# Kernel tuning notes

Hardware: AMD Instinct MI355X
Metric: run time of the kernel (lower is better)

The kernel has to match this reference:

```python
import jax, jax.numpy as jnp
import numpy as np
from jax import lax

B, T, D = 4, 4096, 1024
H = 16                 # n_heads
HD = D // H            # head_dim = 64
NS = 64                # num_slots
SPH = NS // H          # slots_per_head = 4
KPH = 2                # effective per-head top_k = min(max(2, 32//16), 4) = 2
K = KPH * H            # total topk width = 32
HM = 4096              # hidden_mlp


def _p(key, shape, scale=0.02):
    return jax.random.normal(key, shape, dtype=jnp.float32) * scale


def setup_inputs() -> dict:
    key = jax.random.key(0)
    ks = jax.random.split(key, 24)
    return {
        "x": jax.random.normal(ks[0], (B, T, D), dtype=jnp.float32),
        "slot_init": _p(ks[1], (H, SPH, HD)),
        # route_mlp: Linear(2D, D) -> GELU -> Linear(D, NS); weights stored [in, out]
        "rw1": _p(ks[2], (2 * D, D)), "rb1": jnp.zeros((D,), jnp.float32),
        "rw2": _p(ks[3], (D, NS)), "rb2": jnp.zeros((NS,), jnp.float32),
        # GRUCell(HD, HD): torch layout [3*HD, HD]
        "gwi": _p(ks[4], (3 * HD, HD), 0.1), "gwh": _p(ks[5], (3 * HD, HD), 0.1),
        "gbi": jnp.zeros((3 * HD,), jnp.float32), "gbh": jnp.zeros((3 * HD,), jnp.float32),
        # slot_hidden_proj: Linear(HD, 4*HD); slot_out_head: Linear(4*HD, HD)
        "hpw": _p(ks[6], (HD, 4 * HD)), "hpb": jnp.zeros((4 * HD,), jnp.float32),
        "ohw": _p(ks[7], (4 * HD, HD)), "ohb": jnp.zeros((HD,), jnp.float32),
        # slot_value_proj: Linear(D, HM); slot_value_out: Linear(HM, D)
        "vpw": _p(ks[8], (D, HM)), "vpb": jnp.zeros((HM,), jnp.float32),
        "vow": _p(ks[9], (HM, D)), "vob": jnp.zeros((D,), jnp.float32),
        # out_proj: Linear(D, D)
        "opw": _p(ks[10], (D, D)), "opb": jnp.zeros((D,), jnp.float32),
        "tau": jnp.ones((1,), jnp.float32),
    }


def _gelu(x):
    return jax.nn.gelu(x, approximate=False)


def _forward(x, slot_init, rw1, rb1, rw2, rb2, gwi, gwh, gbi, gbh,
             hpw, hpb, ohw, ohb, vpw, vpb, vow, vob, opw, opb, tau):
    # ---- routing ----
    S0 = slot_init.reshape(NS, HD)                     # [NS, HD]
    slot_mean = S0.mean(axis=0)                        # [HD]
    slot_mean_full = jnp.tile(slot_mean, H)            # [D]
    ctx = jnp.concatenate(
        [x, jnp.broadcast_to(slot_mean_full, (B, T, D))], axis=-1)  # [B,T,2D]
    h1 = _gelu(ctx @ rw1 + rb1)
    route_logits = (h1 @ rw2 + rb2) / (jnp.abs(tau[0]) + 0.1)       # [B,T,NS]

    topk_vals, topk_idx = lax.top_k(route_logits, K)   # [B,T,K]
    topk_w = jax.nn.softmax(topk_vals, axis=-1)
    bi = jnp.arange(B)[:, None, None]
    ti = jnp.arange(T)[None, :, None]
    alpha = jnp.zeros((B, T, NS), x.dtype).at[bi, ti, topk_idx].set(topk_w)

    # ---- per-head slot pooling (vectorized over heads) ----
    alpha_h = alpha.reshape(B, T, H, SPH)              # [B,T,H,S]
    x_heads = x.reshape(B, T, H, HD)                   # [B,T,H,HD]
    slot_input = jnp.einsum('bths,bthd->bhsd', alpha_h, x_heads)   # [B,H,S,HD]
    wsum = alpha_h.sum(axis=1) + 1e-8                  # [B,H,S]
    slot_in = slot_input / wsum[..., None]

    # ---- GRU cell update (torch GRUCell semantics) ----
    h_prev = jnp.broadcast_to(slot_init[None], (B, H, SPH, HD))
    gi = slot_in @ gwi.T + gbi                         # [B,H,S,3HD]
    gh = h_prev @ gwh.T + gbh
    ir, iz, in_ = jnp.split(gi, 3, axis=-1)
    hr, hz, hn = jnp.split(gh, 3, axis=-1)
    r = jax.nn.sigmoid(ir + hr)
    z = jax.nn.sigmoid(iz + hz)
    n = jnp.tanh(in_ + r * hn)
    h_new = (1.0 - z) * n + z * h_prev                 # [B,H,S,HD]

    S_new = _gelu(h_new @ hpw + hpb) @ ohw + ohb       # [B,H,S,HD]

    # ---- broadcast back to tokens ----
    out = jnp.einsum('bths,bhsd->bthd', alpha_h, S_new).reshape(B, T, D)
    out = _gelu(out @ vpw + vpb) @ vow + vob
    out = out @ opw + opb
    return out


def reference(x, slot_init, rw1, rb1, rw2, rb2, gwi, gwh, gbi, gbh,
              hpw, hpb, ohw, ohb, vpw, vpb, vow, vob, opw, opb, tau):
    return _forward(x, slot_init, rw1, rb1, rw2, rb2, gwi, gwh, gbi, gbh,
                    hpw, hpb, ohw, ohb, vpw, vpb, vow, vob, opw, opb, tau)
```

## Files before the change

kernel.cpp:

```cpp
#include <hip/hip_runtime.h>
#include <cstddef>
#include <cstdint>

#define Bb 4
#define Tt 4096
#define Dd 1024
#define Hh 16
#define HDd 64
#define NSs 64
#define SPHh 4
#define HMm 4096
#define MTOK (Bb*Tt)

typedef _Float16 f16x8 __attribute__((ext_vector_type(8)));
typedef _Float16 f16x4 __attribute__((ext_vector_type(4)));
typedef float f32x4 __attribute__((ext_vector_type(4)));

__device__ __forceinline__ float gelu_f(float x) {
    return 0.5f * x * (1.0f + erff(x * 0.70710678118654752440f));
}

__device__ __forceinline__ int xcd_swz(int nwg) {
    int orig = blockIdx.y * gridDim.x + blockIdx.x;
    int cpx = nwg >> 3;
    return (orig & 7) * cpx + (orig >> 3);
}

__global__ __launch_bounds__(256) void cb_part_k(const float* __restrict__ slot_init,
                                                 const float* __restrict__ rw1,
                                                 float* __restrict__ cbp) {
    __shared__ float sm[64];
    int tid = threadIdx.x;
    if (tid < 64) {
        float s = 0.f;
        for (int i = 0; i < 64; ++i) s += slot_init[i * 64 + tid];
        sm[tid] = s * (1.0f / 64.0f);
    }
    __syncthreads();
    int j = blockIdx.x * 256 + tid;
    int k0 = blockIdx.y * 64;
    float acc = 0.f;
#pragma unroll 8
    for (int k = 0; k < 64; ++k)
        acc = fmaf(sm[k], rw1[(size_t)(1024 + k0 + k) * 1024 + j], acc);
    cbp[(size_t)blockIdx.y * 1024 + j] = acc;
}

__global__ __launch_bounds__(256) void cb_comb_k(const float* __restrict__ cbp,
                                                 float* __restrict__ cb) {
    int j = blockIdx.x * 256 + threadIdx.x;
    float acc = 0.f;
#pragma unroll
    for (int c = 0; c < 16; ++c) acc += cbp[(size_t)c * 1024 + j];
    cb[j] = acc;
}

__global__ __launch_bounds__(256) void wsplitT_k(const float* __restrict__ rw1,
                                                 _Float16* __restrict__ whiT,
                                                 _Float16* __restrict__ wloT) {
    __shared__ float t[32][33];
    int n0 = blockIdx.x * 32, k0 = blockIdx.y * 32;
    int tx = threadIdx.x & 31, ty = threadIdx.x >> 5;
#pragma unroll
    for (int i = 0; i < 32; i += 8)
        t[ty + i][tx] = rw1[(size_t)(k0 + ty + i) * 1024 + n0 + tx];
    __syncthreads();
#pragma unroll
    for (int i = 0; i < 32; i += 8) {
        float v = t[tx][ty + i];
        _Float16 h = (_Float16)v;
        _Float16 l = (_Float16)(v - (float)h);
        whiT[(size_t)(n0 + ty + i) * 1024 + k0 + tx] = h;
        wloT[(size_t)(n0 + ty + i) * 1024 + k0 + tx] = l;
    }
}

__global__ __launch_bounds__(256) void xsplit_k(const float* __restrict__ x,
                                                _Float16* __restrict__ xhi,
                                                _Float16* __restrict__ xlo) {
    size_t i = ((size_t)blockIdx.x * 256 + threadIdx.x) * 8;
    float4 a = *(const float4*)(x + i);
    float4 b = *(const float4*)(x + i + 4);
    float v[8] = {a.x, a.y, a.z, a.w, b.x, b.y, b.z, b.w};
    f16x8 h, l;
#pragma unroll
    for (int j = 0; j < 8; ++j) {
        _Float16 hv = (_Float16)v[j];
        h[j] = hv;
        l[j] = (_Float16)(v[j] - (float)hv);
    }
    *(f16x8*)(xhi + i) = h;
    *(f16x8*)(xlo + i) = l;
}

__global__ __launch_bounds__(256) void hgemm4_k(const _Float16* __restrict__ Ah,
                                                const _Float16* __restrict__ Al,
                                                const _Float16* __restrict__ Bh,
                                                const _Float16* __restrict__ Bl,
                                                const float* __restrict__ bias1,
                                                const float* __restrict__ bias2,
                                                float* __restrict__ C,
                                                int M, int N, int K) {
    __shared__ __align__(16) _Float16 Ahs[128][32];
    __shared__ __align__(16) _Float16 Als[128][32];
    __shared__ __align__(16) _Float16 Bhs[128][32];
    __shared__ __align__(16) _Float16 Bls[128][32];
    const int tid = threadIdx.x;
    const int wid = tid >> 6;
    const int lane = tid & 63;
    const int swz = xcd_swz(gridDim.x * gridDim.y);
    const int brow = (swz / gridDim.x) * 128;
    const int bcol = (swz % gridDim.x) * 128;
    const int wr = (wid >> 1) * 64;
    const int wc = (wid & 1) * 64;

    const int rb = lane >> 2;
    const int cbk = (lane & 3) * 8;
    const int fr = lane & 15;
    const int fk = (lane >> 4) * 8;

    f32x4 acc[4][4];
#pragma unroll
    for (int m = 0; m < 4; ++m)
#pragma unroll
        for (int n = 0; n < 4; ++n)
            acc[m][n] = f32x4{0.f, 0.f, 0.f, 0.f};

    for (int k0 = 0; k0 < K; k0 += 32) {
#pragma unroll
        for (int i = 0; i < 2; ++i) {
            int r0 = wid * 32 + i * 16;
            const _Float16* gah = Ah + (size_t)(brow + r0 + rb) * K + k0 + cbk;
            __builtin_amdgcn_global_load_lds(
                (const __attribute__((address_space(1))) void*)gah,
                (__attribute__((address_space(3))) void*)&Ahs[r0][0], 16, 0, 0);
            const _Float16* gal = Al + (size_t)(brow + r0 + rb) * K + k0 + cbk;
            __builtin_amdgcn_global_load_lds(
                (const __attribute__((address_space(1))) void*)gal,
                (__attribute__((address_space(3))) void*)&Als[r0][0], 16, 0, 0);
            const _Float16* gbh = Bh + (size_t)(bcol + r0 + rb) * K + k0 + cbk;
            __builtin_amdgcn_global_load_lds(
                (const __attribute__((address_space(1))) void*)gbh,
                (__attribute__((address_space(3))) void*)&Bhs[r0][0], 16, 0, 0);
            const _Float16* gbl = Bl + (size_t)(bcol + r0 + rb) * K + k0 + cbk;
            __builtin_amdgcn_global_load_lds(
                (const __attribute__((address_space(1))) void*)gbl,
                (__attribute__((address_space(3))) void*)&Bls[r0][0], 16, 0, 0);
        }
        __syncthreads();

        f16x8 afh[4], afl[4], bfh[4], bfl[4];
#pragma unroll
        for (int m = 0; m < 4; ++m) {
            afh[m] = *(const f16x8*)&Ahs[wr + m * 16 + fr][fk];
            afl[m] = *(const f16x8*)&Als[wr + m * 16 + fr][fk];
        }
#pragma unroll
        for (int n = 0; n < 4; ++n) {
            bfh[n] = *(const f16x8*)&Bhs[wc + n * 16 + fr][fk];
            bfl[n] = *(const f16x8*)&Bls[wc + n * 16 + fr][fk];
        }
#pragma unroll
        for (int m = 0; m < 4; ++m)
#pragma unroll
            for (int n = 0; n < 4; ++n) {
                acc[m][n] = __builtin_amdgcn_mfma_f32_16x16x32_f16(afl[m], bfh[n], acc[m][n], 0, 0, 0);
                acc[m][n] = __builtin_amdgcn_mfma_f32_16x16x32_f16(afh[m], bfl[n], acc[m][n], 0, 0, 0);
                acc[m][n] = __builtin_amdgcn_mfma_f32_16x16x32_f16(afh[m], bfh[n], acc[m][n], 0, 0, 0);
            }
        __syncthreads();
    }

    const int crow = (lane >> 4) * 4;
#pragma unroll
    for (int m = 0; m < 4; ++m) {
        int row0 = brow + wr + m * 16 + crow;
#pragma unroll
        for (int n = 0; n < 4; ++n) {
            int col = bcol + wc + n * 16 + fr;
            float bv = bias1[col] + bias2[col];
#pragma unroll
            for (int r = 0; r < 4; ++r) {
                float v = acc[m][n][r] + bv;
                C[(size_t)(row0 + r) * N + col] = gelu_f(v);
            }
        }
    }
}

__global__ __launch_bounds__(256) void logits2_k(const float* __restrict__ A,
                                                 const float* __restrict__ Bw,
                                                 const float* __restrict__ rb2,
                                                 const float* __restrict__ taup,
                                                 float* __restrict__ Cl) {
    __shared__ float At[16][68];
    __shared__ float Bs[16][64];
    const int tid = threadIdx.x;
    const int m0 = blockIdx.x * 64;
    const int rg = tid >> 4;
    const int cg = tid & 15;
    const int srow = tid >> 2;
    const int skk  = (tid & 3) * 4;
    const int bk = tid >> 4;
    const int bc = (tid & 15) * 4;

    float acc[4][4] = {};

    for (int k0 = 0; k0 < 1024; k0 += 16) {
        float4 av = *(const float4*)(A + (size_t)(m0 + srow) * 1024 + k0 + skk);
        float4 bv = *(const float4*)(Bw + (size_t)(k0 + bk) * 64 + bc);
        __syncthreads();
        At[skk + 0][srow] = av.x;
        At[skk + 1][srow] = av.y;
        At[skk + 2][srow] = av.z;
        At[skk + 3][srow] = av.w;
        *(float4*)&Bs[bk][bc] = bv;
        __syncthreads();
#pragma unroll
        for (int k = 0; k < 16; ++k) {
            float4 a4 = *(const float4*)&At[k][rg * 4];
            float4 b4 = *(const float4*)&Bs[k][cg * 4];
            float a[4] = {a4.x, a4.y, a4.z, a4.w};
            float b[4] = {b4.x, b4.y, b4.z, b4.w};
#pragma unroll
            for (int i = 0; i < 4; ++i)
#pragma unroll
                for (int j = 0; j < 4; ++j)
                    acc[i][j] = fmaf(a[i], b[j], acc[i][j]);
        }
    }
    float inv = 1.0f / (fabsf(taup[0]) + 0.1f);
#pragma unroll
    for (int i = 0; i < 4; ++i)
#pragma unroll
        for (int j = 0; j < 4; ++j)
            Cl[(size_t)(m0 + rg * 4 + i) * 64 + cg * 4 + j] =
                (acc[i][j] + rb2[cg * 4 + j]) * inv;
}

__global__ __launch_bounds__(256) void topk_k(const float* __restrict__ logits,
                                              float* __restrict__ alpha,
                                              _Float16* __restrict__ alpha16) {
    int wave = threadIdx.x >> 6;
    int lane = threadIdx.x & 63;
    int t = blockIdx.x * 4 + wave;
    float li = logits[(size_t)t * 64 + lane];
    float m = li;
#pragma unroll
    for (int off = 32; off; off >>= 1) m = fmaxf(m, __shfl_xor(m, off, 64));
    int cnt = 0;
    for (int off = 1; off < 64; ++off) {
        int j = (lane + off) & 63;
        float lj = __shfl(li, j, 64);
        cnt += (lj > li) || (lj == li && j < lane);
    }
    float e = (cnt < 32) ? expf(li - m) : 0.0f;
    float s = e;
#pragma unroll
    for (int off = 32; off; off >>= 1) s += __shfl_xor(s, off, 64);
    float a = e / s;
    alpha[(size_t)t * 64 + lane] = a;
    alpha16[(size_t)t * 64 + lane] = (_Float16)a;
}

__global__ __launch_bounds__(256) void pool_part_k(const float* __restrict__ x,
                                                   const float* __restrict__ alpha,
                                                   float* __restrict__ part,
                                                   float* __restrict__ partw) {
    int bh = blockIdx.x;
    int c = blockIdx.y;
    int b = bh >> 4, h = bh & 15;
    int tid = threadIdx.x;
    int s = tid >> 6, d = tid & 63;
    __shared__ float lx[16][64];
    __shared__ float la[16][4];
    float acc = 0.f, wacc = 0.f;
    const int tchunk = Tt / 8;
    const int t0base = c * tchunk;
    for (int t0 = 0; t0 < tchunk; t0 += 16) {
        int ttr = tid >> 4;
        int ddr = (tid & 15) * 4;
        size_t trow = (size_t)b * Tt + t0base + t0 + ttr;
        float4 xv = *(const float4*)(x + trow * Dd + h * 64 + ddr);
        *(float4*)&lx[ttr][ddr] = xv;
        if (tid < 64) {
            int tt2 = tid >> 2, ss = tid & 3;
            la[tt2][ss] = alpha[((size_t)b * Tt + t0base + t0 + tt2) * 64 + h * 4 + ss];
        }
        __syncthreads();
#pragma unroll
        for (int q = 0; q < 16; ++q) {
            float av = la[q][s];
            acc = fmaf(av, lx[q][d], acc);
            wacc += av;
        }
        __syncthreads();
    }
    part[(((size_t)c * 64 + bh) * 4 + s) * 64 + d] = acc;
    if (d == 0) partw[((size_t)c * 64 + bh) * 4 + s] = wacc;
}

__global__ __launch_bounds__(256) void pool_comb_k(const float* __restrict__ part,
                                                   const float* __restrict__ partw,
                                                   float* __restrict__ slot_in) {
    int bh = blockIdx.x;
    int tid = threadIdx.x;
    int s = tid >> 6, d = tid & 63;
    float acc = 0.f, w = 0.f;
    for (int c = 0; c < 8; ++c) {
        acc += part[(((size_t)c * 64 + bh) * 4 + s) * 64 + d];
        w   += partw[((size_t)c * 64 + bh) * 4 + s];
    }
    slot_in[((size_t)bh * 4 + s) * 64 + d] = acc / (w + 1e-8f);
}

__global__ __launch_bounds__(64) void gru_k(const float* __restrict__ slot_in,
                                            const float* __restrict__ slot_init,
                                            const float* __restrict__ gwi,
                                            const float* __restrict__ gwh,
                                            const float* __restrict__ gbi,
                                            const float* __restrict__ gbh,
                                            const float* __restrict__ hpw,
                                            const float* __restrict__ hpb,
                                            const float* __restrict__ ohw,
                                            const float* __restrict__ ohb,
                                            float* __restrict__ S_new) {
    int slot = blockIdx.x;
    int hs = slot & 63;
    int d = threadIdx.x;
    __shared__ float si[64], hp[64], hn[64], g[256];
    si[d] = slot_in[(size_t)slot * 64 + d];
    hp[d] = slot_init[(size_t)hs * 64 + d];
    __syncthreads();
    float gi_r = gbi[d], gi_z = gbi[64 + d], gi_n = gbi[128 + d];
    float gh_r = gbh[d], gh_z = gbh[64 + d], gh_n = gbh[128 + d];
    for (int k = 0; k < 64; ++k) {
        float sv = si[k], hv = hp[k];
        gi_r = fmaf(sv, gwi[(size_t)(d) * 64 + k], gi_r);
        gi_z = fmaf(sv, gwi[(size_t)(64 + d) * 64 + k], gi_z);
        gi_n = fmaf(sv, gwi[(size_t)(128 + d) * 64 + k], gi_n);
        gh_r = fmaf(hv, gwh[(size_t)(d) * 64 + k], gh_r);
        gh_z = fmaf(hv, gwh[(size_t)(64 + d) * 64 + k], gh_z);
        gh_n = fmaf(hv, gwh[(size_t)(128 + d) * 64 + k], gh_n);
    }
    float r = 1.0f / (1.0f + expf(-(gi_r + gh_r)));
    float z = 1.0f / (1.0f + expf(-(gi_z + gh_z)));
    float n = tanhf(gi_n + r * gh_n);
    float hnew = (1.0f - z) * n + z * hp[d];
    hn[d] = hnew;
    __syncthreads();
    float p0 = hpb[d], p1 = hpb[64 + d], p2 = hpb[128 + d], p3 = hpb[192 + d];
    for (int k = 0; k < 64; ++k) {
        float hv = hn[k];
        p0 = fmaf(hv, hpw[(size_t)k * 256 + d], p0);
        p1 = fmaf(hv, hpw[(size_t)k * 256 + 64 + d], p1);
        p2 = fmaf(hv, hpw[(size_t)k * 256 + 128 + d], p2);
        p3 = fmaf(hv, hpw[(size_t)k * 256 + 192 + d], p3);
    }
    g[d] = gelu_f(p0); g[64 + d] = gelu_f(p1); g[128 + d] = gelu_f(p2); g[192 + d] = gelu_f(p3);
    __syncthreads();
    float o = ohb[d];
    for (int j = 0; j < 256; ++j) o = fmaf(g[j], ohw[(size_t)j * 64 + d], o);
    S_new[(size_t)slot * 64 + d] = o;
}

__global__ __launch_bounds__(256) void pmat_k(const float* __restrict__ Snew,
                                              const float* __restrict__ vpw,
                                              _Float16* __restrict__ PT) {
    const int h = blockIdx.y;
    const int tid = threadIdx.x;
    const int j = blockIdx.x * 256 + tid;
    __shared__ float S[16][64];
    for (int i = tid; i < 1024; i += 256) {
        int row = i >> 6, d = i & 63;
        int b = row >> 2, s = row & 3;
        S[row][d] = Snew[((size_t)b * 64 + h * 4 + s) * 64 + d];
    }
    __syncthreads();
    float acc[16];
#pragma unroll
    for (int r = 0; r < 16; ++r) acc[r] = 0.f;
    const float* wp = vpw + (size_t)h * 64 * HMm + j;
#pragma unroll 4
    for (int d = 0; d < 64; ++d) {
        float w = wp[(size_t)d * HMm];
#pragma unroll
        for (int r = 0; r < 16; ++r) acc[r] = fmaf(S[r][d], w, acc[r]);
    }
#pragma unroll
    for (int b = 0; b < 4; ++b) {
        f16x4 o;
#pragma unroll
        for (int s = 0; s < 4; ++s) o[s] = (_Float16)acc[b * 4 + s];
        *(f16x4*)&PT[((size_t)b * HMm + j) * 64 + h * 4] = o;
    }
}

__global__ __launch_bounds__(256) void transp_f16_k(const float* __restrict__ in,
                                                    _Float16* __restrict__ out,
                                                    int K, int N) {
    __shared__ float t[32][33];
    int n0 = blockIdx.x * 32, k0 = blockIdx.y * 32;
    int tx = threadIdx.x & 31, ty = threadIdx.x >> 5;
#pragma unroll
    for (int i = 0; i < 32; i += 8)
        t[ty + i][tx] = in[(size_t)(k0 + ty + i) * N + n0 + tx];
    __syncthreads();
#pragma unroll
    for (int i = 0; i < 32; i += 8)
        out[(size_t)(n0 + ty + i) * K + k0 + tx] = (_Float16)t[tx][ty + i];
}

__global__ __launch_bounds__(256) void vgen_k(const _Float16* __restrict__ alpha16,
                                              const _Float16* __restrict__ PT,
                                              const float* __restrict__ vpb,
                                              _Float16* __restrict__ v1a,
                                              _Float16* __restrict__ v1b) {
    __shared__ __align__(16) _Float16 As[128][64];
    __shared__ __align__(16) _Float16 Bs[128][64];
    const int tid = threadIdx.x;
    const int wid = tid >> 6;
    const int lane = tid & 63;
    const int swz = xcd_swz(gridDim.x * gridDim.y);
    const int brow = (swz / gridDim.x) * 128;
    const int bcol = (swz % gridDim.x) * 128;
    const int b = brow >> 12;
    const _Float16* Bt = PT + (size_t)b * HMm * 64;
    _Float16* Cb = (brow < 8192) ? v1a : v1b;
    const int rowoff = (brow < 8192) ? brow : brow - 8192;
    const int wr = (wid >> 1) * 64;
    const int wc = (wid & 1) * 64;

    f32x4 acc[4][4];
#pragma unroll
    for (int m = 0; m < 4; ++m)
#pragma unroll
        for (int n = 0; n < 4; ++n)
            acc[m][n] = f32x4{0.f, 0.f, 0.f, 0.f};

    const int lrow = lane >> 3;
    const int lcol = (lane & 7) * 8;
    const int fr = lane & 15;
    const int fk = (lane >> 4) * 8;

#pragma unroll
    for (int i = 0; i < 4; ++i) {
        int seg = wid * 4 + i;
        const _Float16* g = alpha16 + (size_t)(brow + seg * 8 + lrow) * 64 + lcol;
        __builtin_amdgcn_global_load_lds(
            (const __attribute__((address_space(1))) void*)g,
            (__attribute__((address_space(3))) void*)&As[seg * 8][0], 16, 0, 0);
    }
#pragma unroll
    for (int i = 0; i < 4; ++i) {
        int seg = wid * 4 + i;
        const _Float16* g = Bt + (size_t)(bcol + seg * 8 + lrow) * 64 + lcol;
        __builtin_amdgcn_global_load_lds(
            (const __attribute__((address_space(1))) void*)g,
            (__attribute__((address_space(3))) void*)&Bs[seg * 8][0], 16, 0, 0);
    }
    __syncthreads();
#pragma unroll
    for (int kb = 0; kb < 2; ++kb) {
        f16x8 af[4], bf[4];
#pragma unroll
        for (int m = 0; m < 4; ++m)
            af[m] = *(const f16x8*)&As[wr + m * 16 + fr][kb * 32 + fk];
#pragma unroll
        for (int n = 0; n < 4; ++n)
            bf[n] = *(const f16x8*)&Bs[wc + n * 16 + fr][kb * 32 + fk];
#pragma unroll
        for (int m = 0; m < 4; ++m)
#pragma unroll
            for (int n = 0; n < 4; ++n)
                acc[m][n] = __builtin_amdgcn_mfma_f32_16x16x32_f16(af[m], bf[n], acc[m][n], 0, 0, 0);
    }

    const int crow = (lane >> 4) * 4;
#pragma unroll
    for (int m = 0; m < 4; ++m) {
        int row0 = rowoff + wr + m * 16 + crow;
#pragma unroll
        for (int n = 0; n < 4; ++n) {
            int col = bcol + wc + n * 16 + fr;
            float bv = vpb[col];
#pragma unroll
            for (int r = 0; r < 4; ++r) {
                float v = acc[m][n][r] + bv;
                Cb[(size_t)(row0 + r) * HMm + col] = (_Float16)gelu_f(v);
            }
        }
    }
}

template <int OUT_F16>
__global__ __launch_bounds__(512, 2) void hgemm8_k(const _Float16* __restrict__ A0,
                                                   const _Float16* __restrict__ A1,
                                                   int splitrow,
                                                   const _Float16* __restrict__ Bt,
                                                   const float* __restrict__ bias,
                                                   void* __restrict__ Cv,
                                                   int M, int N, int K) {
    __shared__ __align__(16) _Float16 As[4][256][32];
    __shared__ __align__(16) _Float16 Bs[4][256][32];
    const int tid = threadIdx.x;
    const int wid = tid >> 6;
    const int lane = tid & 63;
    const int swz = xcd_swz(gridDim.x * gridDim.y);
    const int brow = (swz / gridDim.x) * 256;
    const int bcol = (swz % gridDim.x) * 256;
    const _Float16* Ab = (brow < splitrow) ? A0 : A1;
    const int arow0 = brow - ((brow < splitrow) ? 0 : splitrow);
    const int wm = wid >> 2;
    const int wn = wid & 3;

    const int srow = lane >> 2;
    const int scol = ((lane & 3) ^ ((lane >> 3) & 3)) * 8;
    const int fr = lane & 15;
    const int fkp = (((lane >> 4) ^ ((lane >> 1) & 3))) * 8;
    const int crow = (lane >> 4) * 4;

    const int nk = K >> 5;

    f32x4 acc[8][4];
#pragma unroll
    for (int m = 0; m < 8; ++m)
#pragma unroll
        for (int n = 0; n < 4; ++n)
            acc[m][n] = f32x4{0.f, 0.f, 0.f, 0.f};

    auto stage = [&](int t) {
        const int slot = t & 3;
        const size_t kk = (size_t)t << 5;
#pragma unroll
        for (int i = 0; i < 2; ++i) {
            const _Float16* g = Ab + (size_t)(arow0 + wid * 32 + i * 16 + srow) * K + kk + scol;
            __builtin_amdgcn_global_load_lds(
                (const __attribute__((address_space(1))) void*)g,
                (__attribute__((address_space(3))) void*)&As[slot][wid * 32 + i * 16][0], 16, 0, 0);
        }
#pragma unroll
        for (int i = 0; i < 2; ++i) {
            const _Float16* g = Bt + (size_t)(bcol + wid * 32 + i * 16 + srow) * K + kk + scol;
            __builtin_amdgcn_global_load_lds(
                (const __attribute__((address_space(1))) void*)g,
                (__attribute__((address_space(3))) void*)&Bs[slot][wid * 32 + i * 16][0], 16, 0, 0);
        }
    };

    stage(0);
    if (nk > 1) stage(1);
    if (nk > 2) stage(2);

    for (int t = 0; t < nk; ++t) {
        if (t + 2 < nk)      asm volatile("s_waitcnt vmcnt(8)" ::: "memory");
        else if (t + 1 < nk) asm volatile("s_waitcnt vmcnt(4)" ::: "memory");
        else                 asm volatile("s_waitcnt vmcnt(0)" ::: "memory");
        __builtin_amdgcn_sched_barrier(0);
        __builtin_amdgcn_s_barrier();
        __builtin_amdgcn_sched_barrier(0);

        const int slot = t & 3;
        f16x8 af[8], bf[4];
#pragma unroll
        for (int m = 0; m < 4; ++m)
            af[m] = *(const f16x8*)&As[slot][wm * 128 + m * 16 + fr][fkp];
#pragma unroll
        for (int n = 0; n < 4; ++n)
            bf[n] = *(const f16x8*)&Bs[slot][wn * 64 + n * 16 + fr][fkp];
        if (t + 3 < nk) stage(t + 3);
        __builtin_amdgcn_sched_barrier(0);
        __builtin_amdgcn_s_barrier();
        asm volatile("s_waitcnt lgkmcnt(0)" ::: "memory");
        __builtin_amdgcn_sched_barrier(0);
        __builtin_amdgcn_s_setprio(1);
#pragma unroll
        for (int m = 0; m < 4; ++m)
#pragma unroll
            for (int n = 0; n < 4; ++n)
                acc[m][n] = __builtin_amdgcn_mfma_f32_16x16x32_f16(af[m], bf[n], acc[m][n], 0, 0, 0);
        __builtin_amdgcn_s_setprio(0);
        __builtin_amdgcn_sched_barrier(0);
#pragma unroll
        for (int m = 4; m < 8; ++m)
            af[m] = *(const f16x8*)&As[slot][wm * 128 + m * 16 + fr][fkp];
        __builtin_amdgcn_sched_barrier(0);
        __builtin_amdgcn_s_barrier();
        asm volatile("s_waitcnt lgkmcnt(0)" ::: "memory");
        __builtin_amdgcn_sched_barrier(0);
        __builtin_amdgcn_s_setprio(1);
#pragma unroll
        for (int m = 4; m < 8; ++m)
#pragma unroll
            for (int n = 0; n < 4; ++n)
                acc[m][n] = __builtin_amdgcn_mfma_f32_16x16x32_f16(af[m], bf[n], acc[m][n], 0, 0, 0);
        __builtin_amdgcn_s_setprio(0);
        __builtin_amdgcn_sched_barrier(0);
    }

#pragma unroll
    for (int m = 0; m < 8; ++m) {
        int row0 = brow + wm * 128 + m * 16 + crow;
#pragma unroll
        for (int n = 0; n < 4; ++n) {
            int col = bcol + wn * 64 + n * 16 + fr;
            float bv = bias[col];
#pragma unroll
            for (int r = 0; r < 4; ++r) {
                float v = acc[m][n][r] + bv;
                size_t idx = (size_t)(row0 + r) * N + col;
                if (OUT_F16) ((_Float16*)Cv)[idx] = (_Float16)v;
                else ((float*)Cv)[idx] = v;
            }
        }
    }
    (void)M;
}

extern "C" void kernel_launch(void* const* d_in, const int* in_sizes, int n_in,
                              void* d_out, int out_size, void* d_ws, size_t ws_size,
                              hipStream_t stream) {
    const float* x         = (const float*)d_in[0];
    const float* slot_init = (const float*)d_in[1];
    const float* rw1       = (const float*)d_in[2];
    const float* rb1       = (const float*)d_in[3];
    const float* rw2       = (const float*)d_in[4];
    const float* rb2       = (const float*)d_in[5];
    const float* gwi       = (const float*)d_in[6];
    const float* gwh       = (const float*)d_in[7];
    const float* gbi       = (const float*)d_in[8];
    const float* gbh       = (const float*)d_in[9];
    const float* hpw       = (const float*)d_in[10];
    const float* hpb       = (const float*)d_in[11];
    const float* ohw       = (const float*)d_in[12];
    const float* ohb       = (const float*)d_in[13];
    const float* vpw       = (const float*)d_in[14];
    const float* vpb       = (const float*)d_in[15];
    const float* vow       = (const float*)d_in[16];
    const float* vob       = (const float*)d_in[17];
    const float* opw       = (const float*)d_in[18];
    const float* opb       = (const float*)d_in[19];
    const float* tau       = (const float*)d_in[20];
    float* out = (float*)d_out;

    float* ws = (float*)d_ws;
    size_t off = 0;
    auto alloc = [&](size_t nfloats) { float* p = ws + off; off += (nfloats + 63) & ~(size_t)63; return p; };

    float* cb     = alloc(1024);
    float* cbp    = alloc(16 * 1024);
    float* h1     = alloc((size_t)MTOK * 1024);
    _Float16* v1a = (_Float16*)h1;
    float* logits = alloc((size_t)MTOK * 64);
    float* alpha  = alloc((size_t)MTOK * 64);
    _Float16* alpha16 = (_Float16*)alloc((size_t)MTOK * 64 / 2);
    float* slotin = alloc(256 * 64);
    float* part   = alloc((size_t)8 * 64 * 4 * 64);
    float* partw  = alloc(8 * 64 * 4);
    float* Snew   = alloc(256 * 64);
    _Float16* PT   = (_Float16*)alloc((size_t)Bb * HMm * 64 / 2);
    _Float16* vowT = (_Float16*)alloc((size_t)Dd * HMm / 2);
    _Float16* opwT = (_Float16*)alloc((size_t)Dd * Dd / 2);
    _Float16* v2f16 = (_Float16*)alloc((size_t)MTOK * Dd / 2);
    _Float16* w1hiT = (_Float16*)alloc((size_t)Dd * Dd / 2);
    _Float16* w1loT = (_Float16*)alloc((size_t)Dd * Dd / 2);

    _Float16* xhi = (_Float16*)d_out;
    _Float16* xlo = xhi + (size_t)MTOK * Dd;
    _Float16* v1b = (_Float16*)d_out;

    cb_part_k<<<dim3(4, 16), 256, 0, stream>>>(slot_init, rw1, cbp);
    cb_comb_k<<<4, 256, 0, stream>>>(cbp, cb);
    wsplitT_k<<<dim3(Dd / 32, Dd / 32), 256, 0, stream>>>(rw1, w1hiT, w1loT);
    xsplit_k<<<(MTOK * Dd) / (256 * 8), 256, 0, stream>>>(x, xhi, xlo);
    hgemm4_k<<<dim3(Dd / 128, MTOK / 128), 256, 0, stream>>>(
        xhi, xlo, w1hiT, w1loT, rb1, cb, h1, MTOK, Dd, Dd);
    logits2_k<<<MTOK / 64, 256, 0, stream>>>(h1, rw2, rb2, tau, logits);
    topk_k<<<MTOK / 4, 256, 0, stream>>>(logits, alpha, alpha16);

    transp_f16_k<<<dim3(Dd / 32, HMm / 32), 256, 0, stream>>>(vow, vowT, HMm, Dd);
    transp_f16_k<<<dim3(Dd / 32, Dd / 32), 256, 0, stream>>>(opw, opwT, Dd, Dd);

    pool_part_k<<<dim3(64, 8), 256, 0, stream>>>(x, alpha, part, partw);
    pool_comb_k<<<64, 256, 0, stream>>>(part, partw, slotin);
    gru_k<<<256, 64, 0, stream>>>(slotin, slot_init, gwi, gwh, gbi, gbh,
                                  hpw, hpb, ohw, ohb, Snew);

    pmat_k<<<dim3(HMm / 256, Hh), 256, 0, stream>>>(Snew, vpw, PT);

    vgen_k<<<dim3(HMm / 128, MTOK / 128), 256, 0, stream>>>(
        alpha16, PT, vpb, v1a, v1b);
    hgemm8_k<1><<<dim3(Dd / 256, MTOK / 256), 512, 0, stream>>>(
        v1a, v1b, 8192, vowT, vob, v2f16, MTOK, Dd, HMm);
    hgemm8_k<0><<<dim3(Dd / 256, MTOK / 256), 512, 0, stream>>>(
        v2f16, v2f16, MTOK, opwT, opb, out, MTOK, Dd, Dd);

    (void)in_sizes; (void)n_in; (void)out_size; (void)ws_size;
}
```

Baseline: 563.6 us.

## Rewrite routing split-fp16 GEMM with 256x256 tiles, double-buffered LDS and swizzle

Replaces the 128x128 three-pass split-fp16 routing GEMM with a 512-thread 256x256-tile kernel. It double-buffers LDS loads with explicit vmcnt waits so global loads overlap the MFMA work. It XOR-swizzles the LDS columns to reduce bank conflicts and splits the MFMA phase into two halves, with setprio hints and a prefetch issued between them. The larger tile cuts global traffic per FLOP but raises register and LDS pressure, with 128 KB of LDS per block, and relies on hand-placed barriers and waitcnts being correct.

```diff
diff --git a/kernel.cpp b/kernel.cpp
--- a/kernel.cpp
+++ b/kernel.cpp
@@ -93,73 +93,94 @@
     *(f16x8*)(xlo + i) = l;
 }
 
-__global__ __launch_bounds__(256) void hgemm4_k(const _Float16* __restrict__ Ah,
-                                                const _Float16* __restrict__ Al,
-                                                const _Float16* __restrict__ Bh,
-                                                const _Float16* __restrict__ Bl,
-                                                const float* __restrict__ bias1,
-                                                const float* __restrict__ bias2,
-                                                float* __restrict__ C,
-                                                int M, int N, int K) {
-    __shared__ __align__(16) _Float16 Ahs[128][32];
-    __shared__ __align__(16) _Float16 Als[128][32];
-    __shared__ __align__(16) _Float16 Bhs[128][32];
-    __shared__ __align__(16) _Float16 Bls[128][32];
+__global__ __launch_bounds__(512, 2) void hgemm4p_k(const _Float16* __restrict__ Ah,
+                                                    const _Float16* __restrict__ Al,
+                                                    const _Float16* __restrict__ Bh,
+                                                    const _Float16* __restrict__ Bl,
+                                                    const float* __restrict__ bias1,
+                                                    const float* __restrict__ bias2,
+                                                    float* __restrict__ C,
+                                                    int M, int N, int K) {
+    __shared__ __align__(16) _Float16 Ahs[2][256][32];
+    __shared__ __align__(16) _Float16 Als[2][256][32];
+    __shared__ __align__(16) _Float16 Bhs[2][256][32];
+    __shared__ __align__(16) _Float16 Bls[2][256][32];
     const int tid = threadIdx.x;
     const int wid = tid >> 6;
     const int lane = tid & 63;
     const int swz = xcd_swz(gridDim.x * gridDim.y);
-    const int brow = (swz / gridDim.x) * 128;
-    const int bcol = (swz % gridDim.x) * 128;
-    const int wr = (wid >> 1) * 64;
-    const int wc = (wid & 1) * 64;
-
-    const int rb = lane >> 2;
-    const int cbk = (lane & 3) * 8;
+    const int brow = (swz / gridDim.x) * 256;
+    const int bcol = (swz % gridDim.x) * 256;
+    const int wm = wid >> 2;
+    const int wn = wid & 3;
+
+    const int srow = lane >> 2;
+    const int scol = ((lane & 3) ^ ((lane >> 3) & 3)) * 8;
     const int fr = lane & 15;
-    const int fk = (lane >> 4) * 8;
-
-    f32x4 acc[4][4];
-#pragma unroll
-    for (int m = 0; m < 4; ++m)
+    const int fkp = (((lane >> 4) ^ ((lane >> 1) & 3))) * 8;
+    const int crow = (lane >> 4) * 4;
+
+    const int nk = K >> 5;
+
+    f32x4 acc[8][4];
+#pragma unroll
+    for (int m = 0; m < 8; ++m)
 #pragma unroll
         for (int n = 0; n < 4; ++n)
             acc[m][n] = f32x4{0.f, 0.f, 0.f, 0.f};
 
-    for (int k0 = 0; k0 < K; k0 += 32) {
+    auto stage = [&](int t) {
+        const int slot = t & 1;
+        const size_t kk = (size_t)t << 5;
 #pragma unroll
         for (int i = 0; i < 2; ++i) {
             int r0 = wid * 32 + i * 16;
-            const _Float16* gah = Ah + (size_t)(brow + r0 + rb) * K + k0 + cbk;
+            const _Float16* gah = Ah + (size_t)(brow + r0 + srow) * K + kk + scol;
             __builtin_amdgcn_global_load_lds(
                 (const __attribute__((address_space(1))) void*)gah,
-                (__attribute__((address_space(3))) void*)&Ahs[r0][0], 16, 0, 0);
-            const _Float16* gal = Al + (size_t)(brow + r0 + rb) * K + k0 + cbk;
+                (__attribute__((address_space(3))) void*)&Ahs[slot][r0][0], 16, 0, 0);
+            const _Float16* gal = Al + (size_t)(brow + r0 + srow) * K + kk + scol;
             __builtin_amdgcn_global_load_lds(
                 (const __attribute__((address_space(1))) void*)gal,
-                (__attribute__((address_space(3))) void*)&Als[r0][0], 16, 0, 0);
-            const _Float16* gbh = Bh + (size_t)(bcol + r0 + rb) * K + k0 + cbk;
+                (__attribute__((address_space(3))) void*)&Als[slot][r0][0], 16, 0, 0);
+            const _Float16* gbh = Bh + (size_t)(bcol + r0 + srow) * K + kk + scol;
             __builtin_amdgcn_global_load_lds(
                 (const __attribute__((address_space(1))) void*)gbh,
-                (__attribute__((address_space(3))) void*)&Bhs[r0][0], 16, 0, 0);
-            const _Float16* gbl = Bl + (size_t)(bcol + r0 + rb) * K + k0 + cbk;
+                (__attribute__((address_space(3))) void*)&Bhs[slot][r0][0], 16, 0, 0);
+            const _Float16* gbl = Bl + (size_t)(bcol + r0 + srow) * K + kk + scol;
             __builtin_amdgcn_global_load_lds(
                 (const __attribute__((address_space(1))) void*)gbl,
-                (__attribute__((address_space(3))) void*)&Bls[r0][0], 16, 0, 0);
-        }
-        __syncthreads();
-
-        f16x8 afh[4], afl[4], bfh[4], bfl[4];
+                (__attribute__((address_space(3))) void*)&Bls[slot][r0][0], 16, 0, 0);
+        }
+    };
+
+    stage(0);
+    if (nk > 1) stage(1);
+
+    for (int t = 0; t < nk; ++t) {
+        if (t + 1 < nk) asm volatile("s_waitcnt vmcnt(8)" ::: "memory");
+        else            asm volatile("s_waitcnt vmcnt(0)" ::: "memory");
+        __builtin_amdgcn_sched_barrier(0);
+        __builtin_amdgcn_s_barrier();
+        __builtin_amdgcn_sched_barrier(0);
+
+        const int slot = t & 1;
+        f16x8 afh[8], afl[8], bfh[4], bfl[4];
 #pragma unroll
         for (int m = 0; m < 4; ++m) {
-            afh[m] = *(const f16x8*)&Ahs[wr + m * 16 + fr][fk];
-            afl[m] = *(const f16x8*)&Als[wr + m * 16 + fr][fk];
+            afh[m] = *(const f16x8*)&Ahs[slot][wm * 128 + m * 16 + fr][fkp];
+            afl[m] = *(const f16x8*)&Als[slot][wm * 128 + m * 16 + fr][fkp];
         }
 #pragma unroll
         for (int n = 0; n < 4; ++n) {
-            bfh[n] = *(const f16x8*)&Bhs[wc + n * 16 + fr][fk];
-            bfl[n] = *(const f16x8*)&Bls[wc + n * 16 + fr][fk];
-        }
+            bfh[n] = *(const f16x8*)&Bhs[slot][wn * 64 + n * 16 + fr][fkp];
+            bfl[n] = *(const f16x8*)&Bls[slot][wn * 64 + n * 16 + fr][fkp];
+        }
+        __builtin_amdgcn_sched_barrier(0);
+        __builtin_amdgcn_s_barrier();
+        asm volatile("s_waitcnt lgkmcnt(0)" ::: "memory");
+        __builtin_amdgcn_sched_barrier(0);
+        __builtin_amdgcn_s_setprio(1);
 #pragma unroll
         for (int m = 0; m < 4; ++m)
 #pragma unroll
@@ -168,16 +189,37 @@
                 acc[m][n] = __builtin_amdgcn_mfma_f32_16x16x32_f16(afh[m], bfl[n], acc[m][n], 0, 0, 0);
                 acc[m][n] = __builtin_amdgcn_mfma_f32_16x16x32_f16(afh[m], bfh[n], acc[m][n], 0, 0, 0);
             }
-        __syncthreads();
-    }
-
-    const int crow = (lane >> 4) * 4;
-#pragma unroll
-    for (int m = 0; m < 4; ++m) {
-        int row0 = brow + wr + m * 16 + crow;
+        __builtin_amdgcn_s_setprio(0);
+        __builtin_amdgcn_sched_barrier(0);
+#pragma unroll
+        for (int m = 4; m < 8; ++m) {
+            afh[m] = *(const f16x8*)&Ahs[slot][wm * 128 + m * 16 + fr][fkp];
+            afl[m] = *(const f16x8*)&Als[slot][wm * 128 + m * 16 + fr][fkp];
+        }
+        asm volatile("s_waitcnt lgkmcnt(0)" ::: "memory");
+        __builtin_amdgcn_sched_barrier(0);
+        __builtin_amdgcn_s_barrier();
+        __builtin_amdgcn_sched_barrier(0);
+        if (t + 2 < nk) stage(t + 2);
+        __builtin_amdgcn_s_setprio(1);
+#pragma unroll
+        for (int m = 4; m < 8; ++m)
+#pragma unroll
+            for (int n = 0; n < 4; ++n) {
+                acc[m][n] = __builtin_amdgcn_mfma_f32_16x16x32_f16(afl[m], bfh[n], acc[m][n], 0, 0, 0);
+                acc[m][n] = __builtin_amdgcn_mfma_f32_16x16x32_f16(afh[m], bfl[n], acc[m][n], 0, 0, 0);
+                acc[m][n] = __builtin_amdgcn_mfma_f32_16x16x32_f16(afh[m], bfh[n], acc[m][n], 0, 0, 0);
+            }
+        __builtin_amdgcn_s_setprio(0);
+        __builtin_amdgcn_sched_barrier(0);
+    }
+
+#pragma unroll
+    for (int m = 0; m < 8; ++m) {
+        int row0 = brow + wm * 128 + m * 16 + crow;
 #pragma unroll
         for (int n = 0; n < 4; ++n) {
-            int col = bcol + wc + n * 16 + fr;
+            int col = bcol + wn * 64 + n * 16 + fr;
             float bv = bias1[col] + bias2[col];
 #pragma unroll
             for (int r = 0; r < 4; ++r) {
@@ -186,6 +228,7 @@
             }
         }
     }
+    (void)M;
 }
 
 __global__ __launch_bounds__(256) void logits2_k(const float* __restrict__ A,
@@ -673,7 +716,7 @@
     cb_comb_k<<<4, 256, 0, stream>>>(cbp, cb);
     wsplitT_k<<<dim3(Dd / 32, Dd / 32), 256, 0, stream>>>(rw1, w1hiT, w1loT);
     xsplit_k<<<(MTOK * Dd) / (256 * 8), 256, 0, stream>>>(x, xhi, xlo);
-    hgemm4_k<<<dim3(Dd / 128, MTOK / 128), 256, 0, stream>>>(
+    hgemm4p_k<<<dim3(Dd / 256, MTOK / 256), 512, 0, stream>>>(
         xhi, xlo, w1hiT, w1loT, rb1, cb, h1, MTOK, Dd, Dd);
     logits2_k<<<MTOK / 64, 256, 0, stream>>>(h1, rw2, rb2, tau, logits);
     topk_k<<<MTOK / 4, 256, 0, stream>>>(logits, alpha, alpha16);
```

Result: faster. 545.8 us (-3.2%).
